# Kernel optimization log

Measured on AMD Instinct MI355X. Metric: run time of the kernel, lower is better.

## Reference

```python
import jax, jax.numpy as jnp
import numpy as np

D = 1280
RANK = 4

def _lora(x, down, up):
    # x: [..., in]; down: [r, in]; up: [out, r]
    return (x @ down.T) @ up.T

def setup_inputs() -> dict:
    key = jax.random.key(0)
    ks = jax.random.split(key, 15)
    B, S = 4, 2048
    inp = {
        'hidden_states': jax.random.normal(ks[0], (B, S, D), jnp.float32),
        'Wq': jax.random.normal(ks[1], (D, D), jnp.float32) * (D ** -0.5),
        'Wk': jax.random.normal(ks[2], (D, D), jnp.float32) * (D ** -0.5),
        'Wv': jax.random.normal(ks[3], (D, D), jnp.float32) * (D ** -0.5),
        'Wo': jax.random.normal(ks[4], (D, D), jnp.float32) * (D ** -0.5),
        'bo': jax.random.normal(ks[5], (D,), jnp.float32) * 0.02,
        'q_down': jax.random.normal(ks[6], (RANK, D), jnp.float32) / RANK,
        'q_up': jax.random.normal(ks[7], (D, RANK), jnp.float32) * 0.02,
        'k_down': jax.random.normal(ks[8], (RANK, D), jnp.float32) / RANK,
        'k_up': jax.random.normal(ks[9], (D, RANK), jnp.float32) * 0.02,
        'v_down': jax.random.normal(ks[10], (RANK, D), jnp.float32) / RANK,
        'v_up': jax.random.normal(ks[11], (D, RANK), jnp.float32) * 0.02,
        'o_down': jax.random.normal(ks[12], (RANK, D), jnp.float32) / RANK,
        'o_up': jax.random.normal(ks[13], (D, RANK), jnp.float32) * 0.02,
        'num_heads': 8,
    }
    return inp

def reference(hidden_states, Wq, Wk, Wv, Wo, bo, q_down, q_up, k_down, k_up,
              v_down, v_up, o_down, o_up, num_heads):
    B, S, Dm = hidden_states.shape
    H = num_heads
    hd = Dm // H
    scale = hd ** -0.5
    x = hidden_states
    # base projections + rank-4 LoRA deltas (self-attention: enc == x)
    q = x @ Wq.T + _lora(x, q_down, q_up)
    k = x @ Wk.T + _lora(x, k_down, k_up)
    v = x @ Wv.T + _lora(x, v_down, v_up)
    q = q.reshape(B, S, H, hd)
    k = k.reshape(B, S, H, hd)
    v = v.reshape(B, S, H, hd)
    # explicit bmm -> softmax -> bmm attention (no mask, no norm_cross)
    scores = jnp.einsum('bqhd,bkhd->bhqk', q, k) * scale  # [B,H,S,S]
    probs = jax.nn.softmax(scores, axis=-1)
    ctx = jnp.einsum('bhqk,bkhd->bqhd', probs, v).reshape(B, S, Dm)
    # output projection (with bias) + LoRA on output; dropout is identity at eval
    out = ctx @ Wo.T + bo + _lora(ctx, o_down, o_up)
    return out
```

## Files before the change

### kernel.cpp

```cpp
#include <hip/hip_runtime.h>
#include <cstdint>

typedef _Float16 f16;
typedef f16 f16x8 __attribute__((ext_vector_type(8)));
typedef f16 f16x4 __attribute__((ext_vector_type(4)));
typedef f16 f16x2 __attribute__((ext_vector_type(2)));
typedef float f32x4 __attribute__((ext_vector_type(4)));
typedef uint32_t u32x4 __attribute__((ext_vector_type(4)));

#define D_MODEL 1280
#define SEQ 2048
#define BATCH 4
#define HEADS 8
#define HDIM 160
#define MTOT (BATCH*SEQ)
#define NQKV (3*D_MODEL)

__device__ __forceinline__ void gload_lds16(const f16* g, f16* l) {
  __builtin_amdgcn_global_load_lds(
      (const __attribute__((address_space(1))) unsigned int*)g,
      (__attribute__((address_space(3))) unsigned int*)l,
      16, 0, 0);
}

#define BARX() { asm volatile("" ::: "memory"); __builtin_amdgcn_s_barrier(); asm volatile("" ::: "memory"); }
#define VMW(N) { asm volatile("s_waitcnt vmcnt(" #N ")" ::: "memory"); }


__global__ void convert_f32_to_f16(const float* __restrict__ in, f16* __restrict__ out, int n4) {
  int i = blockIdx.x * 256 + threadIdx.x;
  if (i < n4) {
    float4 v = ((const float4*)in)[i];
    f16x4 o = { (f16)v.x, (f16)v.y, (f16)v.z, (f16)v.w };
    ((f16x4*)out)[i] = o;
  }
}

__global__ void build_weff(const float* __restrict__ W, const float* __restrict__ up,
                           const float* __restrict__ down, f16* __restrict__ out) {
  int idx = blockIdx.x * 256 + threadIdx.x;
  int o  = idx / (D_MODEL / 4);
  int i0 = (idx % (D_MODEL / 4)) * 4;
  float4 w = *(const float4*)&W[(size_t)o * D_MODEL + i0];
  float u0 = up[o*4+0], u1 = up[o*4+1], u2 = up[o*4+2], u3 = up[o*4+3];
  float vals[4] = { w.x, w.y, w.z, w.w };
  f16x4 r;
#pragma unroll
  for (int j = 0; j < 4; ++j) {
    int i = i0 + j;
    float acc = vals[j] + u0*down[i] + u1*down[D_MODEL + i]
                        + u2*down[2*D_MODEL + i] + u3*down[3*D_MODEL + i];
    r[j] = (f16)acc;
  }
  *(f16x4*)&out[(size_t)o * D_MODEL + i0] = r;
}

__global__ void transpose_v(const f16* __restrict__ qkv, f16* __restrict__ Vt) {
  __shared__ f16 t[32][33];
  int s0 = blockIdx.x * 32;
  int d0 = blockIdx.y * 32;
  int bh = blockIdx.z;
  int b = bh >> 3, h = bh & 7;
  int j = threadIdx.x & 31;
  int i0 = threadIdx.x >> 5;
#pragma unroll
  for (int k = 0; k < 4; ++k) {
    int i = i0 + k * 8;
    t[i][j] = qkv[(size_t)(b*SEQ + s0 + i) * NQKV + 2*D_MODEL + h*HDIM + d0 + j];
  }
  __syncthreads();
  int sj = (((j>>2) ^ (j>>3)) & 1) ? (j ^ 12) : j;
#pragma unroll
  for (int k = 0; k < 4; ++k) {
    int i = i0 + k * 8;
    Vt[(size_t)(bh*HDIM + d0 + i) * SEQ + s0 + sj] = t[j][i];
  }
}

__global__ __launch_bounds__(512) void gemm256(const f16* __restrict__ A,
                                               const f16* __restrict__ Bw,
                                               f16* __restrict__ C) {
  const int K = D_MODEL, ldc = NQKV, NT = D_MODEL/64;
  __shared__ alignas(16) f16 lds[7 * 8192];
  f16* LB = lds + 3*8192;
  int tid = threadIdx.x;
  int wv = tid >> 6, l = tid & 63;
  int wm = wv >> 2, wn = wv & 3;
  int lr = l & 15, lg = l >> 4;
  int bm = blockIdx.y, bn = blockIdx.x;

  int row0 = tid >> 3;
  int csw  = ((tid & 7) ^ (row0 & 7)) * 8;
  const f16* Asrc[2]; const f16* Bsrc[2];
#pragma unroll
  for (int h = 0; h < 2; ++h) {
    Asrc[h] = A  + (size_t)(bm*256 + h*128 + row0) * K + csw;
    Bsrc[h] = Bw + (size_t)(bn*256 + h*128 + row0) * K + csw;
  }
  int ldsoff = wv * 512;

  int xsl0 = ((lg)     ^ (lr & 7)) * 8;
  int xsl1 = ((4 + lg) ^ (lr & 7)) * 8;

  f32x4 acc[8][4] = {};

#define STAGE_A(h, slot, kt) { const f16* s_ = Asrc[h] + (kt)*64; f16* d_ = lds + (slot)*8192 + ldsoff; \
    gload_lds16(s_, d_); gload_lds16(s_ + (size_t)64*K, d_ + 4096); }
#define STAGE_B(h, slot, kt) { const f16* s_ = Bsrc[h] + (kt)*64; f16* d_ = LB + (slot)*8192 + ldsoff; \
    gload_lds16(s_, d_); gload_lds16(s_ + (size_t)64*K, d_ + 4096); }

  STAGE_A(0, 0, 0); STAGE_A(1, 1, 0);
  STAGE_B(0, 0, 0); STAGE_B(1, 1, 0);
  STAGE_B(0, 2, 1);
  VMW(2); BARX();

  for (int t = 0; t < NT; ++t) {
    int sA0 = (2*t) % 3, sA1 = (2*t+1) % 3, sA2 = (2*t+2) % 3;
    int sB0 = (2*t) & 3, sB1 = (2*t+1) & 3, sB3 = (2*t+3) & 3;
    int tc1 = (t+1 < NT) ? t+1 : NT-1;
    int tc2 = (t+2 < NT) ? t+2 : NT-1;

#define PHASE(ah, bh, sA, sB, STG, VMOPT) { \
    f16x8 af[4][2], bf[2][2]; \
    _Pragma("unroll") \
    for (int j = 0; j < 4; ++j) { \
      int base = (sA)*8192 + (wm*64 + j*16 + lr)*64; \
      af[j][0] = *(const f16x8*)&lds[base + xsl0]; \
      af[j][1] = *(const f16x8*)&lds[base + xsl1]; \
    } \
    _Pragma("unroll") \
    for (int i = 0; i < 2; ++i) { \
      int base = (sB)*8192 + (wn*32 + i*16 + lr)*64; \
      bf[i][0] = *(const f16x8*)&LB[base + xsl0]; \
      bf[i][1] = *(const f16x8*)&LB[base + xsl1]; \
    } \
    STG; \
    BARX(); \
    __builtin_amdgcn_s_setprio(1); \
    _Pragma("unroll") \
    for (int j = 0; j < 4; ++j) \
      _Pragma("unroll") \
      for (int i = 0; i < 2; ++i) { \
        acc[(ah)*4+j][(bh)*2+i] = __builtin_amdgcn_mfma_f32_16x16x32_f16(af[j][0], bf[i][0], acc[(ah)*4+j][(bh)*2+i], 0, 0, 0); \
        acc[(ah)*4+j][(bh)*2+i] = __builtin_amdgcn_mfma_f32_16x16x32_f16(af[j][1], bf[i][1], acc[(ah)*4+j][(bh)*2+i], 0, 0, 0); \
      } \
    __builtin_amdgcn_s_setprio(0); \
    VMOPT; \
    BARX(); }

    PHASE(0, 0, sA0, sB0, STAGE_B(1, sB3, tc1), VMW(2))
    PHASE(1, 0, sA1, sB0, STAGE_A(0, sA2, tc1), )
    PHASE(0, 1, sA0, sB1, STAGE_B(0, sB0, tc2), )
    PHASE(1, 1, sA1, sB1, STAGE_A(1, sA0, tc1), VMW(4))
#undef PHASE
  }

#pragma unroll
  for (int mf = 0; mf < 8; ++mf) {
    int r0 = bm*256 + (mf>>2)*128 + wm*64 + (mf&3)*16 + lg*4;
#pragma unroll
    for (int nf = 0; nf < 4; ++nf) {
      int c = bn*256 + (nf>>1)*128 + wn*32 + (nf&1)*16 + lr;
#pragma unroll
      for (int rg = 0; rg < 4; ++rg)
        C[(size_t)(r0 + rg) * ldc + c] = (f16)acc[mf][nf][rg];
    }
  }
#undef STAGE_A
#undef STAGE_B
}


template<int OUTF16>
__global__ __launch_bounds__(256) void gemm_bt(
    const f16* __restrict__ A, int lda,
    const f16* __restrict__ Bw,
    void* __restrict__ Cp, int ldc,
    const float* __restrict__ bias,
    int N, int K) {
  __shared__ alignas(16) f16 As[128 * 32];
  __shared__ alignas(16) f16 Bs[128 * 32];
  int tid = threadIdx.x;
  int w = tid >> 6, l = tid & 63;
  int wm = w >> 1, wn = w & 1;
  int bm = blockIdx.y, bn = blockIdx.x;
  int lr = l & 15, lg = l >> 4;

  f32x4 acc[4][4] = {};

  const int srow = w * 32 + (l >> 2);
  const int scol = (l & 3) * 8;
  const f16* Ab = A  + (size_t)(bm*128 + srow) * lda + scol;
  const f16* Bb = Bw + (size_t)(bn*128 + srow) * K   + scol;
  f16* AsW = &As[w * 1024];
  f16* BsW = &Bs[w * 1024];

  for (int k0 = 0; k0 < K; k0 += 32) {
    gload_lds16(Ab + k0,                     AsW);
    gload_lds16(Ab + k0 + (size_t)16 * lda,  AsW + 512);
    gload_lds16(Bb + k0,                     BsW);
    gload_lds16(Bb + k0 + (size_t)16 * K,    BsW + 512);
    __syncthreads();
    f16x8 af[4], bf[4];
#pragma unroll
    for (int f = 0; f < 4; ++f) {
      af[f] = *(const f16x8*)&As[(wm*64 + f*16 + lr) * 32 + lg * 8];
      bf[f] = *(const f16x8*)&Bs[(wn*64 + f*16 + lr) * 32 + lg * 8];
    }
    __builtin_amdgcn_s_setprio(1);
#pragma unroll
    for (int fr = 0; fr < 4; ++fr)
#pragma unroll
      for (int fc = 0; fc < 4; ++fc)
        acc[fr][fc] = __builtin_amdgcn_mfma_f32_16x16x32_f16(af[fr], bf[fc], acc[fr][fc], 0, 0, 0);
    __builtin_amdgcn_s_setprio(0);
    __syncthreads();
  }

#pragma unroll
  for (int fr = 0; fr < 4; ++fr) {
    int r0 = bm*128 + wm*64 + fr*16 + lg*4;
#pragma unroll
    for (int fc = 0; fc < 4; ++fc) {
      int c = bn*128 + wn*64 + fc*16 + lr;
#pragma unroll
      for (int rg = 0; rg < 4; ++rg) {
        size_t off = (size_t)(r0 + rg) * ldc + c;
        if (OUTF16) ((f16*)Cp)[off] = (f16)acc[fr][fc][rg];
        else        ((float*)Cp)[off] = acc[fr][fc][rg] + bias[c];
      }
    }
  }
}

__global__ __launch_bounds__(256, 2) void attn(const f16* __restrict__ qkv,
                                               const f16* __restrict__ Vt,
                                               f16* __restrict__ ctx) {
  __shared__ alignas(16) f16 Kl[64 * 168];
  __shared__ alignas(16) f16 Vl[160 * 64];
  int tid = threadIdx.x;
  int wv = tid >> 6, l = tid & 63;
  int lr = l & 15, lg = l >> 4;
  int qt = blockIdx.x, bh = blockIdx.y;
  int b = bh >> 3, h = bh & 7;
  size_t qrow[2];
#pragma unroll
  for (int qg = 0; qg < 2; ++qg)
    qrow[qg] = (size_t)(b*SEQ + qt*128 + wv*32 + qg*16 + lr);

  const f16 qscale = (f16)0.114055069f;
  f16x8 qf[2][5];
#pragma unroll
  for (int qg = 0; qg < 2; ++qg)
#pragma unroll
    for (int dk = 0; dk < 5; ++dk) {
      f16x8 t = *(const f16x8*)&qkv[qrow[qg] * NQKV + h*HDIM + dk*32 + lg*8];
#pragma unroll
      for (int j = 0; j < 8; ++j) t[j] = t[j] * qscale;
      qf[qg][dk] = t;
    }

  const char* Kg0 = (const char*)qkv + (size_t)(b*SEQ)*NQKV*2 + (size_t)D_MODEL*2 + (size_t)h*HDIM*2;
  char* KlB = (char*)Kl;
  uint32_t koff[6];
  f16* kld[6];
#pragma unroll
  for (int it = 0; it < 6; ++it) {
    int p = (it < 5) ? it*256 + tid : 1280 + (tid & 63);
    koff[it] = (uint32_t)(p/21) * (NQKV*2) + (uint32_t)(p%21) * 16;
    kld[it] = (f16*)(KlB + ((it < 5) ? (it*256 + wv*64)*16 : 1280*16));
  }

  const char* Vg0 = (const char*)Vt + (size_t)bh*HDIM*SEQ*2;
  char* VlB = (char*)Vl;
  uint32_t voff[5];
  f16* vld[5];
#pragma unroll
  for (int it = 0; it < 5; ++it) {
    int c = it*256 + tid;
    int row = c >> 3, sp = c & 7;
    voff[it] = (uint32_t)row * (SEQ*2) + (uint32_t)((sp ^ (row & 7)) * 16);
    vld[it] = (f16*)(VlB + (it*256 + wv*64)*16);
  }
  uint32_t vro[2];
#pragma unroll
  for (int ks = 0; ks < 2; ++ks)
    vro[ks] = (uint32_t)lr*128 + (uint32_t)((((ks*4+lg) ^ (lr & 7)) * 16));

  f32x4 oacc[10][2] = {};
  float m[2] = {-1e30f, -1e30f}, lsum[2] = {0.f, 0.f};

  for (int kt = 0; kt < 32; ++kt) {
    const char* Ksrc = Kg0 + (size_t)kt * (64*NQKV*2);
    const char* Vsrc = Vg0 + (size_t)kt * 128;
#pragma unroll
    for (int it = 0; it < 5; ++it) {
      gload_lds16((const f16*)(Ksrc + koff[it]), kld[it]);
      gload_lds16((const f16*)(Vsrc + voff[it]), vld[it]);
    }
    if (wv == 0)
      gload_lds16((const f16*)(Ksrc + koff[5]), kld[5]);
    __syncthreads();

    f32x4 sc[4][2] = {};
    __builtin_amdgcn_s_setprio(1);
#pragma unroll
    for (int kb = 0; kb < 4; ++kb)
#pragma unroll
      for (int dk = 0; dk < 5; ++dk) {
        f16x8 a = *(const f16x8*)&Kl[(kb*16 + lr)*168 + dk*32 + lg*8];
        sc[kb][0] = __builtin_amdgcn_mfma_f32_16x16x32_f16(a, qf[0][dk], sc[kb][0], 0, 0, 0);
        sc[kb][1] = __builtin_amdgcn_mfma_f32_16x16x32_f16(a, qf[1][dk], sc[kb][1], 0, 0, 0);
      }
    __builtin_amdgcn_s_setprio(0);

    float smax[2];
#pragma unroll
    for (int qg = 0; qg < 2; ++qg) {
      float sm = -1e30f;
#pragma unroll
      for (int kb = 0; kb < 4; ++kb)
#pragma unroll
        for (int rg = 0; rg < 4; ++rg) sm = fmaxf(sm, sc[kb][qg][rg]);
      sm = fmaxf(sm, __shfl_xor(sm, 16));
      sm = fmaxf(sm, __shfl_xor(sm, 32));
      smax[qg] = sm;
    }
    if (!__all(fmaxf(smax[0] - m[0], smax[1] - m[1]) <= 11.54f)) {
#pragma unroll
      for (int qg = 0; qg < 2; ++qg) {
        float mn = fmaxf(m[qg], smax[qg]);
        float alpha = exp2f(m[qg] - mn);
#pragma unroll
        for (int df = 0; df < 10; ++df)
#pragma unroll
          for (int rg = 0; rg < 4; ++rg) oacc[df][qg][rg] *= alpha;
        lsum[qg] *= alpha;
        m[qg] = mn;
      }
    }

    f16x8 pb[2][2];
#pragma unroll
    for (int qg = 0; qg < 2; ++qg) {
      float ps[16];
      float psum = 0.f;
#pragma unroll
      for (int kb = 0; kb < 4; ++kb)
#pragma unroll
        for (int rg = 0; rg < 4; ++rg) {
          float p = exp2f(sc[kb][qg][rg] - m[qg]);
          ps[kb*4 + rg] = p;
          psum += p;
        }
      psum += __shfl_xor(psum, 16);
      psum += __shfl_xor(psum, 32);
      lsum[qg] += psum;

      uint32_t w0, w1, w2, w3, w4, w5, w6, w7;
      asm("v_cvt_pkrtz_f16_f32 %0, %1, %2" : "=v"(w0) : "v"(ps[0]),  "v"(ps[1]));
      asm("v_cvt_pkrtz_f16_f32 %0, %1, %2" : "=v"(w1) : "v"(ps[2]),  "v"(ps[3]));
      asm("v_cvt_pkrtz_f16_f32 %0, %1, %2" : "=v"(w2) : "v"(ps[4]),  "v"(ps[5]));
      asm("v_cvt_pkrtz_f16_f32 %0, %1, %2" : "=v"(w3) : "v"(ps[6]),  "v"(ps[7]));
      asm("v_cvt_pkrtz_f16_f32 %0, %1, %2" : "=v"(w4) : "v"(ps[8]),  "v"(ps[9]));
      asm("v_cvt_pkrtz_f16_f32 %0, %1, %2" : "=v"(w5) : "v"(ps[10]), "v"(ps[11]));
      asm("v_cvt_pkrtz_f16_f32 %0, %1, %2" : "=v"(w6) : "v"(ps[12]), "v"(ps[13]));
      asm("v_cvt_pkrtz_f16_f32 %0, %1, %2" : "=v"(w7) : "v"(ps[14]), "v"(ps[15]));
      asm("v_permlane32_swap_b32 %0, %1" : "+v"(w0), "+v"(w2));
      asm("v_permlane32_swap_b32 %0, %1" : "+v"(w1), "+v"(w3));
      asm("v_permlane32_swap_b32 %0, %1" : "+v"(w4), "+v"(w6));
      asm("v_permlane32_swap_b32 %0, %1" : "+v"(w5), "+v"(w7));
      u32x4 c0 = { w0, w1, w2, w3 };
      u32x4 c1 = { w4, w5, w6, w7 };
      pb[qg][0] = __builtin_bit_cast(f16x8, c0);
      pb[qg][1] = __builtin_bit_cast(f16x8, c1);
    }

    __builtin_amdgcn_s_setprio(1);
#pragma unroll
    for (int df = 0; df < 10; ++df)
#pragma unroll
      for (int ks = 0; ks < 2; ++ks) {
        f16x8 a = *(const f16x8*)(VlB + vro[ks] + df*2048);
        oacc[df][0] = __builtin_amdgcn_mfma_f32_16x16x32_f16(a, pb[0][ks], oacc[df][0], 0, 0, 0);
        oacc[df][1] = __builtin_amdgcn_mfma_f32_16x16x32_f16(a, pb[1][ks], oacc[df][1], 0, 0, 0);
      }
    __builtin_amdgcn_s_setprio(0);
    __syncthreads();
  }

#pragma unroll
  for (int qg = 0; qg < 2; ++qg) {
    float inv = 1.f / lsum[qg];
#pragma unroll
    for (int df = 0; df < 10; ++df)
#pragma unroll
      for (int pr = 0; pr < 2; ++pr) {
        f16x2 pv = { (f16)(oacc[df][qg][pr*2+0] * inv), (f16)(oacc[df][qg][pr*2+1] * inv) };
        *(f16x2*)&ctx[qrow[qg] * D_MODEL + h*HDIM + df*16 + lg*4 + pr*2] = pv;
      }
  }
}


extern "C" void kernel_launch(void* const* d_in, const int* in_sizes, int n_in,
                              void* d_out, int out_size, void* d_ws, size_t ws_size,
                              hipStream_t stream) {
  const float* x   = (const float*)d_in[0];
  const float* Wq  = (const float*)d_in[1];
  const float* Wk  = (const float*)d_in[2];
  const float* Wv  = (const float*)d_in[3];
  const float* Wo  = (const float*)d_in[4];
  const float* bo  = (const float*)d_in[5];
  const float* q_down = (const float*)d_in[6];
  const float* q_up   = (const float*)d_in[7];
  const float* k_down = (const float*)d_in[8];
  const float* k_up   = (const float*)d_in[9];
  const float* v_down = (const float*)d_in[10];
  const float* v_up   = (const float*)d_in[11];
  const float* o_down = (const float*)d_in[12];
  const float* o_up   = (const float*)d_in[13];
  float* out = (float*)d_out;

  char* ws = (char*)d_ws;
  f16* xh    = (f16*)ws;
  f16* Wqkv  = (f16*)(ws + 20971520);
  f16* WoE   = (f16*)(ws + 20971520 + 9830400);
  f16* qkv   = (f16*)(ws + 20971520 + 9830400 + 3276800);
  f16* Vt    = (f16*)(ws + 20971520 + 9830400 + 3276800 + 62914560);
  f16* ctx   = xh;

  convert_f32_to_f16<<<(MTOT*D_MODEL/4 + 255)/256, 256, 0, stream>>>(x, xh, MTOT*D_MODEL/4);
  build_weff<<<D_MODEL*D_MODEL/4/256, 256, 0, stream>>>(Wq, q_up, q_down, Wqkv);
  build_weff<<<D_MODEL*D_MODEL/4/256, 256, 0, stream>>>(Wk, k_up, k_down, Wqkv + (size_t)D_MODEL*D_MODEL);
  build_weff<<<D_MODEL*D_MODEL/4/256, 256, 0, stream>>>(Wv, v_up, v_down, Wqkv + (size_t)2*D_MODEL*D_MODEL);
  build_weff<<<D_MODEL*D_MODEL/4/256, 256, 0, stream>>>(Wo, o_up, o_down, WoE);

  gemm256<<<dim3(NQKV/256, MTOT/256), 512, 0, stream>>>(xh, Wqkv, qkv);
  transpose_v<<<dim3(SEQ/32, HDIM/32, BATCH*HEADS), 256, 0, stream>>>(qkv, Vt);
  attn<<<dim3(SEQ/128, BATCH*HEADS), 256, 0, stream>>>(qkv, Vt, ctx);
  gemm_bt<0><<<dim3(D_MODEL/128, MTOT/128), 256, 0, stream>>>(ctx, D_MODEL, WoE, out, D_MODEL,
                                                              bo, D_MODEL, D_MODEL);
  (void)in_sizes; (void)n_in; (void)out_size; (void)ws_size;
}
```

Before: 290.0 us.

## Use pipelined 256-tile GEMM for output projection, add XCD-aware block remap

Drops the simple 128-tile gemm_bt and runs the output projection through the pipelined 256x256 gemm256 kernel, templated to write fp32 with bias. Adds an XCD-aware block index remap to gemm256 and attn so that neighbouring tiles sharing operands land on the same chiplet's L2. It also vectorises the V transpose to 4-wide loads and stores. The output GEMM grid shrinks to 5x32 = 160 blocks, which may underfill the GPU. The remap assumes the grid divides evenly by 8.

```diff
diff --git a/kernel.cpp b/kernel.cpp
--- a/kernel.cpp
+++ b/kernel.cpp
@@ -56,38 +56,49 @@
 }
 
 __global__ void transpose_v(const f16* __restrict__ qkv, f16* __restrict__ Vt) {
-  __shared__ f16 t[32][33];
+  __shared__ f16 t[32][36];
   int s0 = blockIdx.x * 32;
   int d0 = blockIdx.y * 32;
   int bh = blockIdx.z;
   int b = bh >> 3, h = bh & 7;
-  int j = threadIdx.x & 31;
-  int i0 = threadIdx.x >> 5;
-#pragma unroll
-  for (int k = 0; k < 4; ++k) {
-    int i = i0 + k * 8;
-    t[i][j] = qkv[(size_t)(b*SEQ + s0 + i) * NQKV + 2*D_MODEL + h*HDIM + d0 + j];
+  int tid = threadIdx.x;
+  {
+    int i = tid >> 3, j4 = (tid & 7) * 4;
+    *(f16x4*)&t[i][j4] =
+        *(const f16x4*)&qkv[(size_t)(b*SEQ + s0 + i) * NQKV + 2*D_MODEL + h*HDIM + d0 + j4];
   }
   __syncthreads();
-  int sj = (((j>>2) ^ (j>>3)) & 1) ? (j ^ 12) : j;
-#pragma unroll
-  for (int k = 0; k < 4; ++k) {
-    int i = i0 + k * 8;
-    Vt[(size_t)(bh*HDIM + d0 + i) * SEQ + s0 + sj] = t[j][i];
-  }
-}
-
+  {
+    int dd = tid >> 3, s4 = (tid & 7) * 4;
+    f16x4 v;
+#pragma unroll
+    for (int k = 0; k < 4; ++k) {
+      int s = s4 + k;
+      int sj = (((s>>2) ^ (s>>3)) & 1) ? (s ^ 12) : s;
+      v[k] = t[sj][dd];
+    }
+    *(f16x4*)&Vt[(size_t)(bh*HDIM + d0 + dd) * SEQ + s0 + s4] = v;
+  }
+}
+
+template<int OUTF32>
 __global__ __launch_bounds__(512) void gemm256(const f16* __restrict__ A,
                                                const f16* __restrict__ Bw,
-                                               f16* __restrict__ C) {
-  const int K = D_MODEL, ldc = NQKV, NT = D_MODEL/64;
+                                               void* __restrict__ Cp, int ldc,
+                                               const float* __restrict__ bias) {
+  const int K = D_MODEL, NT = D_MODEL/64;
   __shared__ alignas(16) f16 lds[7 * 8192];
   f16* LB = lds + 3*8192;
   int tid = threadIdx.x;
   int wv = tid >> 6, l = tid & 63;
   int wm = wv >> 2, wn = wv & 3;
   int lr = l & 15, lg = l >> 4;
-  int bm = blockIdx.y, bn = blockIdx.x;
+
+  int flat = blockIdx.y * gridDim.x + blockIdx.x;
+  int bnn = gridDim.x;
+  int xcd = flat & 7, idx = flat >> 3;
+  int bm = xcd * 4 + idx / bnn;
+  int bn = idx % bnn;
 
   int row0 = tid >> 3;
   int csw  = ((tid & 7) ^ (row0 & 7)) * 8;
@@ -161,76 +172,20 @@
 #pragma unroll
     for (int nf = 0; nf < 4; ++nf) {
       int c = bn*256 + (nf>>1)*128 + wn*32 + (nf&1)*16 + lr;
-#pragma unroll
-      for (int rg = 0; rg < 4; ++rg)
-        C[(size_t)(r0 + rg) * ldc + c] = (f16)acc[mf][nf][rg];
+      if constexpr (OUTF32) {
+        float bb = bias[c];
+#pragma unroll
+        for (int rg = 0; rg < 4; ++rg)
+          ((float*)Cp)[(size_t)(r0 + rg) * ldc + c] = acc[mf][nf][rg] + bb;
+      } else {
+#pragma unroll
+        for (int rg = 0; rg < 4; ++rg)
+          ((f16*)Cp)[(size_t)(r0 + rg) * ldc + c] = (f16)acc[mf][nf][rg];
+      }
     }
   }
 #undef STAGE_A
 #undef STAGE_B
-}
-
-
-template<int OUTF16>
-__global__ __launch_bounds__(256) void gemm_bt(
-    const f16* __restrict__ A, int lda,
-    const f16* __restrict__ Bw,
-    void* __restrict__ Cp, int ldc,
-    const float* __restrict__ bias,
-    int N, int K) {
-  __shared__ alignas(16) f16 As[128 * 32];
-  __shared__ alignas(16) f16 Bs[128 * 32];
-  int tid = threadIdx.x;
-  int w = tid >> 6, l = tid & 63;
-  int wm = w >> 1, wn = w & 1;
-  int bm = blockIdx.y, bn = blockIdx.x;
-  int lr = l & 15, lg = l >> 4;
-
-  f32x4 acc[4][4] = {};
-
-  const int srow = w * 32 + (l >> 2);
-  const int scol = (l & 3) * 8;
-  const f16* Ab = A  + (size_t)(bm*128 + srow) * lda + scol;
-  const f16* Bb = Bw + (size_t)(bn*128 + srow) * K   + scol;
-  f16* AsW = &As[w * 1024];
-  f16* BsW = &Bs[w * 1024];
-
-  for (int k0 = 0; k0 < K; k0 += 32) {
-    gload_lds16(Ab + k0,                     AsW);
-    gload_lds16(Ab + k0 + (size_t)16 * lda,  AsW + 512);
-    gload_lds16(Bb + k0,                     BsW);
-    gload_lds16(Bb + k0 + (size_t)16 * K,    BsW + 512);
-    __syncthreads();
-    f16x8 af[4], bf[4];
-#pragma unroll
-    for (int f = 0; f < 4; ++f) {
-      af[f] = *(const f16x8*)&As[(wm*64 + f*16 + lr) * 32 + lg * 8];
-      bf[f] = *(const f16x8*)&Bs[(wn*64 + f*16 + lr) * 32 + lg * 8];
-    }
-    __builtin_amdgcn_s_setprio(1);
-#pragma unroll
-    for (int fr = 0; fr < 4; ++fr)
-#pragma unroll
-      for (int fc = 0; fc < 4; ++fc)
-        acc[fr][fc] = __builtin_amdgcn_mfma_f32_16x16x32_f16(af[fr], bf[fc], acc[fr][fc], 0, 0, 0);
-    __builtin_amdgcn_s_setprio(0);
-    __syncthreads();
-  }
-
-#pragma unroll
-  for (int fr = 0; fr < 4; ++fr) {
-    int r0 = bm*128 + wm*64 + fr*16 + lg*4;
-#pragma unroll
-    for (int fc = 0; fc < 4; ++fc) {
-      int c = bn*128 + wn*64 + fc*16 + lr;
-#pragma unroll
-      for (int rg = 0; rg < 4; ++rg) {
-        size_t off = (size_t)(r0 + rg) * ldc + c;
-        if (OUTF16) ((f16*)Cp)[off] = (f16)acc[fr][fc][rg];
-        else        ((float*)Cp)[off] = acc[fr][fc][rg] + bias[c];
-      }
-    }
-  }
 }
 
 __global__ __launch_bounds__(256, 2) void attn(const f16* __restrict__ qkv,
@@ -241,7 +196,10 @@
   int tid = threadIdx.x;
   int wv = tid >> 6, l = tid & 63;
   int lr = l & 15, lg = l >> 4;
-  int qt = blockIdx.x, bh = blockIdx.y;
+  int flat = blockIdx.y * 16 + blockIdx.x;
+  int xcd = flat & 7, idx = flat >> 3;
+  int bh = xcd * 4 + (idx >> 4);
+  int qt = idx & 15;
   int b = bh >> 3, h = bh & 7;
   size_t qrow[2];
 #pragma unroll
@@ -436,10 +394,9 @@
   build_weff<<<D_MODEL*D_MODEL/4/256, 256, 0, stream>>>(Wv, v_up, v_down, Wqkv + (size_t)2*D_MODEL*D_MODEL);
   build_weff<<<D_MODEL*D_MODEL/4/256, 256, 0, stream>>>(Wo, o_up, o_down, WoE);
 
-  gemm256<<<dim3(NQKV/256, MTOT/256), 512, 0, stream>>>(xh, Wqkv, qkv);
+  gemm256<0><<<dim3(NQKV/256, MTOT/256), 512, 0, stream>>>(xh, Wqkv, qkv, NQKV, nullptr);
   transpose_v<<<dim3(SEQ/32, HDIM/32, BATCH*HEADS), 256, 0, stream>>>(qkv, Vt);
   attn<<<dim3(SEQ/128, BATCH*HEADS), 256, 0, stream>>>(qkv, Vt, ctx);
-  gemm_bt<0><<<dim3(D_MODEL/128, MTOT/128), 256, 0, stream>>>(ctx, D_MODEL, WoE, out, D_MODEL,
-                                                              bo, D_MODEL, D_MODEL);
+  gemm256<1><<<dim3(D_MODEL/256, MTOT/256), 512, 0, stream>>>(ctx, WoE, out, D_MODEL, bo);
   (void)in_sizes; (void)n_in; (void)out_size; (void)ws_size;
 }
```

Result: faster. 282.5 us (-2.6%).
